# Performance work log

Hardware: AMD Instinct MI355X
Metric: run time of the kernel (lower is better)

Reference implementation:

```python
import jax, jax.numpy as jnp
import numpy as np

B, S, D = 4, 4096, 512
HEADS, NS, NEXT = 8, 32, 2048
HD = D // HEADS
SCALE = 1.0 / np.sqrt(HD)


def setup_inputs() -> dict:
    key = jax.random.key(0)
    ks = jax.random.split(key, 12)
    w_scale = 1.0 / np.sqrt(D)
    return {
        "sequence_tokens": jax.random.normal(ks[0], (B, S, D), jnp.float32),
        "sequence_mask": jnp.ones((B, S), dtype=bool),
        "ns_tokens": jax.random.normal(ks[1], (B, NS, D), jnp.float32),
        "ns_mask": jnp.ones((B, NS), dtype=bool),
        "next_sequence_length": NEXT,
        "Wq": jax.random.normal(ks[2], (D, D), jnp.float32) * w_scale,
        "Wk": jax.random.normal(ks[3], (D, D), jnp.float32) * w_scale,
        "Wv": jax.random.normal(ks[4], (D, D), jnp.float32) * w_scale,
        "ns_q_w": jax.random.normal(ks[5], (NS, D, D), jnp.float32) * w_scale,
        "ns_k_w": jax.random.normal(ks[6], (NS, D, D), jnp.float32) * w_scale,
        "ns_v_w": jax.random.normal(ks[7], (NS, D, D), jnp.float32) * w_scale,
        "Wo": jax.random.normal(ks[8], (D, D), jnp.float32) * w_scale,
    }


def reference(sequence_tokens, sequence_mask, ns_tokens, ns_mask,
              next_sequence_length, Wq, Wk, Wv, ns_q_w, ns_k_w, ns_v_w, Wo):
    b, s, d = sequence_tokens.shape
    ns = ns_tokens.shape[1]
    nxt = next_sequence_length

    seq_q = sequence_tokens[:, -nxt:]
    seq_q_mask = sequence_mask[:, -nxt:]

    # mixed projections: standard linear for seq tokens, per-position weights for NS tokens
    q = jnp.concatenate([seq_q @ Wq.T,
                         jnp.einsum('bnd,ndo->bno', ns_tokens, ns_q_w)], axis=1)
    k = jnp.concatenate([sequence_tokens @ Wk.T,
                         jnp.einsum('bnd,ndo->bno', ns_tokens, ns_k_w)], axis=1)
    v = jnp.concatenate([sequence_tokens @ Wv.T,
                         jnp.einsum('bnd,ndo->bno', ns_tokens, ns_v_w)], axis=1)

    def heads(x):  # [b, t, d] -> [b, h, t, hd]
        return x.reshape(b, -1, HEADS, HD).transpose(0, 2, 1, 3)
    q, k, v = heads(q), heads(k), heads(v)

    total = s + ns
    q_pos = jnp.concatenate([jnp.arange(s - nxt, s), jnp.arange(s, total)])
    k_pos = jnp.arange(total)
    causal = k_pos[None, :] <= q_pos[:, None]              # [Q, K]
    key_mask = jnp.concatenate([sequence_mask, ns_mask], axis=1)  # [b, K]

    logits = jnp.einsum('bhqd,bhkd->bhqk',
                        q.astype(jnp.float32), k.astype(jnp.float32)) * SCALE
    logits = jnp.where(causal[None, None], logits, -10000.0)
    logits = jnp.where(key_mask[:, None, None, :], logits, -10000.0)
    w = jax.nn.softmax(logits, axis=-1).astype(q.dtype)

    att = jnp.einsum('bhqk,bhkd->bhqd', w, v)
    att = att.transpose(0, 2, 1, 3).reshape(b, nxt + ns, d)
    att = att @ Wo.T

    seq_out = att[:, :nxt] * seq_q_mask[..., None].astype(att.dtype)
    ns_out = att[:, nxt:] * ns_mask[..., None].astype(att.dtype)
    return (seq_out, ns_out)
```

## Files before the change

### kernel.cpp

```cpp
#include <hip/hip_runtime.h>

#define NBATCH 4
#define SEQ    4096
#define DMODEL 512
#define NHEAD  8
#define HDIM   64
#define NSN    32
#define NXT    2048
#define QLEN   2080
#define KLEN   4128

using bf16x8 = __attribute__((ext_vector_type(8))) short;
using f32x4  = __attribute__((ext_vector_type(4))) float;

typedef __attribute__((address_space(1))) unsigned int gu32;
typedef __attribute__((address_space(3))) unsigned int lu32;

#define QSCALE 0.18033688f

__device__ __forceinline__ unsigned short f2bf(float f) {
  unsigned int u = __float_as_uint(f);
  u += 0x7FFF + ((u >> 16) & 1);
  return (unsigned short)(u >> 16);
}

__device__ __forceinline__ float bf2f(unsigned short u) {
  return __uint_as_float((unsigned int)u << 16);
}

__device__ __forceinline__ f32x4 mfma16(bf16x8 a, bf16x8 b, f32x4 c) {
  return __builtin_amdgcn_mfma_f32_16x16x32_bf16(a, b, c, 0, 0, 0);
}

__device__ __forceinline__ void gload_lds16(const void* g, void* lds_base) {
  __builtin_amdgcn_global_load_lds((const gu32*)g, (lu32*)lds_base, 16, 0, 0);
}

__device__ __forceinline__ unsigned int cvt_pk_bf16(float lo, float hi) {
  unsigned int r;
  asm("v_cvt_pk_bf16_f32 %0, %1, %2" : "=v"(r) : "v"(lo), "v"(hi));
  return r;
}

__global__ __launch_bounds__(256) void cvt_f32_bf16_v4(const float* __restrict__ src,
                                                       unsigned short* __restrict__ dst, int n4) {
  int i = blockIdx.x * 256 + threadIdx.x;
  if (i >= n4) return;
  float4 v = reinterpret_cast<const float4*>(src)[i];
  ushort4 r;
  r.x = f2bf(v.x); r.y = f2bf(v.y); r.z = f2bf(v.z); r.w = f2bf(v.w);
  reinterpret_cast<ushort4*>(dst)[i] = r;
}

__global__ __launch_bounds__(256) void cvt_w4(const float* __restrict__ a, const float* __restrict__ b,
                                              const float* __restrict__ c, const float* __restrict__ d,
                                              unsigned short* __restrict__ dst) {
  const float* s = blockIdx.y == 0 ? a : blockIdx.y == 1 ? b : blockIdx.y == 2 ? c : d;
  int i = blockIdx.x * 256 + threadIdx.x;
  float4 v = reinterpret_cast<const float4*>(s)[i];
  ushort4 r;
  r.x = f2bf(v.x); r.y = f2bf(v.y); r.z = f2bf(v.z); r.w = f2bf(v.w);
  reinterpret_cast<ushort4*>(dst)[(size_t)blockIdx.y * 65536 + i] = r;
}

__global__ __launch_bounds__(256) void proj_gemm(const unsigned short* __restrict__ X,
                                                 const unsigned short* __restrict__ W,
                                                 unsigned short* __restrict__ Out,
                                                 int rpb_shift, int row_off, int out_L, float scale) {
  __shared__ unsigned short As[128 * 32];
  __shared__ unsigned short Bs[128 * 32];
  const int tid = threadIdx.x;
  const int w = tid >> 6, l = tid & 63;
  const int lg = l >> 4, lr = l & 15;
  const int row0 = blockIdx.x * 128, col0 = blockIdx.y * 128;
  const int wr = (w >> 1) * 64, wc = (w & 1) * 64;
  const int mask = (1 << rpb_shift) - 1;

  f32x4 acc[4][4];
#pragma unroll
  for (int m = 0; m < 4; ++m)
#pragma unroll
    for (int n = 0; n < 4; ++n) acc[m][n] = (f32x4){0.f, 0.f, 0.f, 0.f};

  const int sr = w * 16 + (l >> 2);
  const int sc = (l & 3) * 8;

  for (int k0 = 0; k0 < 512; k0 += 32) {
#pragma unroll
    for (int i = 0; i < 2; ++i) {
      int gr = row0 + sr + i * 64;
      int xrow = ((gr >> rpb_shift) << 12) + row_off + (gr & mask);
      const unsigned short* gpa = X + (size_t)xrow * 512 + k0 + sc;
      gload_lds16(gpa, (char*)As + i * 4096 + w * 1024);
      const unsigned short* gpb = W + (size_t)(col0 + sr + i * 64) * 512 + k0 + sc;
      gload_lds16(gpb, (char*)Bs + i * 4096 + w * 1024);
    }
    __syncthreads();
    bf16x8 av[4], bv[4];
#pragma unroll
    for (int m = 0; m < 4; ++m) av[m] = *(const bf16x8*)&As[(wr + m * 16 + lr) * 32 + lg * 8];
#pragma unroll
    for (int n = 0; n < 4; ++n) bv[n] = *(const bf16x8*)&Bs[(wc + n * 16 + lr) * 32 + lg * 8];
#pragma unroll
    for (int m = 0; m < 4; ++m)
#pragma unroll
      for (int n = 0; n < 4; ++n) acc[m][n] = mfma16(av[m], bv[n], acc[m][n]);
    __syncthreads();
  }

#pragma unroll
  for (int m = 0; m < 4; ++m) {
    int crow = row0 + wr + m * 16 + lg * 4;
#pragma unroll
    for (int n = 0; n < 4; ++n) {
      int ccol = col0 + wc + n * 16 + lr;
      int hh = ccol >> 6, dd = ccol & 63;
#pragma unroll
      for (int r = 0; r < 4; ++r) {
        int cr = crow + r;
        int bb = cr >> rpb_shift, ii = cr & mask;
        Out[(((size_t)bb * NHEAD + hh) * out_L + ii) * HDIM + dd] = f2bf(acc[m][n][r] * scale);
      }
    }
  }
}

__global__ __launch_bounds__(256) void ns_proj(const float* __restrict__ nst,
                                               const float* __restrict__ Wnq, const float* __restrict__ Wnk,
                                               const float* __restrict__ Wnv,
                                               unsigned short* __restrict__ Qb, unsigned short* __restrict__ Kb,
                                               unsigned short* __restrict__ Vb) {
  const int oc = blockIdx.x, n = blockIdx.y, p = blockIdx.z;
  const float* W = p == 0 ? Wnq : p == 1 ? Wnk : Wnv;
  unsigned short* Out = p == 0 ? Qb : p == 1 ? Kb : Vb;
  const int out_L = p == 0 ? QLEN : KLEN;
  const int orow = p == 0 ? NXT + n : SEQ + n;
  const float scale = p == 0 ? QSCALE : 1.f;

  __shared__ float xs[NBATCH][DMODEL];
  __shared__ float red[NBATCH][128];
  const int tid = threadIdx.x;
  for (int idx = tid; idx < NBATCH * DMODEL; idx += 256)
    xs[idx >> 9][idx & 511] = nst[(size_t)((idx >> 9) * NSN + n) * DMODEL + (idx & 511)];
  __syncthreads();

  const int o = oc * 128 + (tid & 127);
  const int dh = tid >> 7;
  float a0 = 0.f, a1 = 0.f, a2 = 0.f, a3 = 0.f;
  const float* wp = W + (size_t)n * DMODEL * DMODEL + o;
#pragma unroll 8
  for (int d = dh * 256; d < dh * 256 + 256; ++d) {
    float wv = wp[(size_t)d * DMODEL];
    a0 += xs[0][d] * wv; a1 += xs[1][d] * wv; a2 += xs[2][d] * wv; a3 += xs[3][d] * wv;
  }
  if (dh == 1) { red[0][tid & 127] = a0; red[1][tid & 127] = a1; red[2][tid & 127] = a2; red[3][tid & 127] = a3; }
  __syncthreads();
  if (dh == 0) {
    a0 += red[0][tid & 127]; a1 += red[1][tid & 127]; a2 += red[2][tid & 127]; a3 += red[3][tid & 127];
    int hh = o >> 6, dd = o & 63;
    float v[4] = {a0, a1, a2, a3};
#pragma unroll
    for (int b = 0; b < NBATCH; ++b)
      Out[(((size_t)b * NHEAD + hh) * out_L + orow) * HDIM + dd] = f2bf(v[b] * scale);
  }
}

__global__ __launch_bounds__(256) void vtrans(const unsigned short* __restrict__ V,
                                              unsigned short* __restrict__ Vt) {
  __shared__ unsigned short t[64 * 64];
  const int tid = threadIdx.x;
  const int kv0 = blockIdx.x * 64, bh = blockIdx.y;
  const unsigned short* Vhp = V + (size_t)bh * KLEN * HDIM;
  unsigned short* Vtp = Vt + (size_t)bh * HDIM * KLEN;

#pragma unroll
  for (int i = 0; i < 2; ++i) {
    int c = i * 256 + tid;
    int row = c >> 3, c8 = c & 7;
    int kvg = kv0 + row; if (kvg > KLEN - 1) kvg = KLEN - 1;
    int4 v4 = *(const int4*)(Vhp + (size_t)kvg * HDIM + c8 * 8);
    *(int4*)&t[row * 64 + ((c8 ^ ((row >> 3) & 7)) * 8)] = v4;
  }
  __syncthreads();
#pragma unroll
  for (int i = 0; i < 2; ++i) {
    int c = i * 256 + tid;
    int d = c >> 3, k8 = c & 7;
    if (kv0 + k8 * 8 <= KLEN - 8) {
      unsigned int wd[4];
#pragma unroll
      for (int jj = 0; jj < 4; ++jj) {
        int ka = k8 * 8 + jj * 2, kb2 = ka + 1;
        unsigned int lo = t[ka  * 64 + (((d >> 3) ^ ((ka  >> 3) & 7)) * 8) + (d & 7)];
        unsigned int hi = t[kb2 * 64 + (((d >> 3) ^ ((kb2 >> 3) & 7)) * 8) + (d & 7)];
        wd[jj] = lo | (hi << 16);
      }
      int4 o; o.x = wd[0]; o.y = wd[1]; o.z = wd[2]; o.w = wd[3];
      *(int4*)(Vtp + (size_t)d * KLEN + kv0 + k8 * 8) = o;
    }
  }
}

__global__ __launch_bounds__(256) void attn_kernel(const unsigned short* __restrict__ Qb,
                                                   const unsigned short* __restrict__ Kb,
                                                   const unsigned short* __restrict__ Vtg,
                                                   unsigned short* __restrict__ PoA,
                                                   float2* __restrict__ PmlA,
                                                   unsigned short* __restrict__ PoB,
                                                   float2* __restrict__ PmlB) {
  __shared__ unsigned short Ks[64 * 64];
  __shared__ unsigned short Vs[64 * 64];

  const int tid = threadIdx.x;
  const int w = tid >> 6, l = tid & 63;
  const int lg = l >> 4, lr = l & 15;
  const bool geven = (l & 16) == 0;
  const int bx = (int)blockIdx.x;
  const int qb = 32 - bx / 3;
  const int sp = bx - 3 * (32 - qb);
  const int bh = (int)blockIdx.z * NHEAD + (int)blockIdx.y;
  const int q0 = qb * 64;
  const int base = NXT + q0;
  const int nkb = (base >> 6) + 1;
  const int t0 = (sp * nkb) / 3;
  const int t1 = ((sp + 1) * nkb) / 3;

  const unsigned short* Qh = Qb + (size_t)bh * QLEN * HDIM;
  const unsigned short* Kh = Kb + (size_t)bh * KLEN * HDIM;
  const unsigned short* Vh = Vtg + (size_t)bh * HDIM * KLEN;

  int qrow = q0 + w * 16 + lr; if (qrow > QLEN - 1) qrow = QLEN - 1;
  const bf16x8 qa0 = *(const bf16x8*)(Qh + (size_t)qrow * HDIM + lg * 8);
  const bf16x8 qa1 = *(const bf16x8*)(Qh + (size_t)qrow * HDIM + 32 + lg * 8);

  f32x4 acc[4];
#pragma unroll
  for (int n = 0; n < 4; ++n) acc[n] = (f32x4){0.f, 0.f, 0.f, 0.f};
  float m_r = 0.f, lsum = 0.f;

  const bf16x8 ones = {(short)0x3F80, (short)0x3F80, (short)0x3F80, (short)0x3F80,
                       (short)0x3F80, (short)0x3F80, (short)0x3F80, (short)0x3F80};

  const int rloc = l >> 3;
  const int jsrc = ((l & 7) ^ rloc) * 8;

  for (int kb = t0; kb < t1; ++kb) {
    const int kv0 = kb * 64;
    if (kv0 + 64 <= KLEN) {
#pragma unroll
      for (int i = 0; i < 2; ++i) {
        const int r8 = (w * 2 + i) * 8;
        gload_lds16(Kh + (size_t)(kv0 + r8 + rloc) * HDIM + jsrc, &Ks[r8 * 64]);
        gload_lds16(Vh + (size_t)(r8 + rloc) * KLEN + kv0 + jsrc, &Vs[r8 * 64]);
      }
    } else {
#pragma unroll
      for (int i = 0; i < 2; ++i) {
        const int r8 = (w * 2 + i) * 8;
        int kr = kv0 + r8 + rloc; if (kr > KLEN - 1) kr = KLEN - 1;
        gload_lds16(Kh + (size_t)kr * HDIM + jsrc, &Ks[r8 * 64]);
        int vc = kv0 + jsrc; if (vc > KLEN - 8) vc = KLEN - 8;
        gload_lds16(Vh + (size_t)(r8 + rloc) * KLEN + vc, &Vs[r8 * 64]);
      }
    }
    __syncthreads();

    const f32x4 minit = {-m_r, -m_r, -m_r, -m_r};
    f32x4 s[4];
#pragma unroll
    for (int n = 0; n < 4; ++n) {
      const int rk = n * 16 + lr;
      const bf16x8 k0 = *(const bf16x8*)&Ks[rk * 64 + ((lg ^ (rk & 7)) * 8)];
      const bf16x8 k1 = *(const bf16x8*)&Ks[rk * 64 + (((4 + lg) ^ (rk & 7)) * 8)];
      s[n] = mfma16(k0, qa0, minit);
      s[n] = mfma16(k1, qa1, s[n]);
    }

    if (kb == nkb - 1) {
      const int qk_lim = base + w * 16 + lr;
#pragma unroll
      for (int n = 0; n < 4; ++n)
#pragma unroll
        for (int r = 0; r < 4; ++r)
          if (kv0 + n * 16 + lg * 4 + r > qk_lim) s[n][r] = -1e30f;
    }

    float a3 = fmaxf(fmaxf(s[0][0], s[0][1]), s[0][2]);
    float b3 = fmaxf(fmaxf(s[0][3], s[1][0]), s[1][1]);
    float c3 = fmaxf(fmaxf(s[1][2], s[1][3]), s[2][0]);
    float d3 = fmaxf(fmaxf(s[2][1], s[2][2]), s[2][3]);
    float e3 = fmaxf(fmaxf(s[3][0], s[3][1]), s[3][2]);
    float rl = fmaxf(fmaxf(a3, b3), c3);
    rl = fmaxf(fmaxf(rl, d3), e3);
    rl = fmaxf(rl, s[3][3]);

    if (__any(rl > 11.5f)) {
      float rmax = fmaxf(rl, __shfl_xor(rl, 16));
      rmax = fmaxf(rmax, __shfl_xor(rmax, 32));
      float dl = fmaxf(rmax, 0.f);
      float sc = exp2f(-dl);
      lsum *= sc; m_r += dl;
#pragma unroll
      for (int n = 0; n < 4; ++n) {
        acc[n][0] *= sc; acc[n][1] *= sc; acc[n][2] *= sc; acc[n][3] *= sc;
#pragma unroll
        for (int r = 0; r < 4; ++r) s[n][r] = exp2f(s[n][r] - dl);
      }
    } else {
#pragma unroll
      for (int n = 0; n < 4; ++n)
#pragma unroll
        for (int r = 0; r < 4; ++r) s[n][r] = exp2f(s[n][r]);
    }

    unsigned int wpk[4][2];
#pragma unroll
    for (int n = 0; n < 4; ++n) {
      wpk[n][0] = cvt_pk_bf16(s[n][0], s[n][1]);
      wpk[n][1] = cvt_pk_bf16(s[n][2], s[n][3]);
    }
    bf16x8 pb[2];
#pragma unroll
    for (int ks = 0; ks < 2; ++ks) {
      unsigned int A0 = wpk[2 * ks][0], B0 = wpk[2 * ks + 1][0];
      unsigned int A1 = wpk[2 * ks][1], B1 = wpk[2 * ks + 1][1];
      asm("v_permlane32_swap_b32 %0, %1" : "+v"(A0), "+v"(B0));
      asm("v_permlane32_swap_b32 %0, %1" : "+v"(A1), "+v"(B1));
      unsigned int sA0 = __builtin_amdgcn_ds_swizzle(A0, 0x401F);
      unsigned int sA1 = __builtin_amdgcn_ds_swizzle(A1, 0x401F);
      unsigned int sB0 = __builtin_amdgcn_ds_swizzle(B0, 0x401F);
      unsigned int sB1 = __builtin_amdgcn_ds_swizzle(B1, 0x401F);
      int4 words;
      words.x = geven ? A0 : sB0;
      words.y = geven ? A1 : sB1;
      words.z = geven ? sA0 : B0;
      words.w = geven ? sA1 : B1;
      pb[ks] = *(bf16x8*)&words;
    }

    f32x4 acc_s = (f32x4){0.f, 0.f, 0.f, 0.f};
    acc_s = mfma16(ones, pb[0], acc_s);
    acc_s = mfma16(ones, pb[1], acc_s);
    lsum += acc_s[0];

#pragma unroll
    for (int n = 0; n < 4; ++n) {
      const int rv = n * 16 + lr;
#pragma unroll
      for (int ks = 0; ks < 2; ++ks) {
        const bf16x8 vv = *(const bf16x8*)&Vs[rv * 64 + (((ks * 4 + lg) ^ (rv & 7)) * 8)];
        acc[n] = mfma16(vv, pb[ks], acc[n]);
      }
    }

    __syncthreads();
  }

  const int qi = q0 + w * 16 + lr;
  if (qi < QLEN) {
    unsigned short* po; float2* pml; size_t rowp;
    if (sp < 2) { rowp = (size_t)(sp * 32 + bh) * QLEN + qi; po = PoA + rowp * 64; pml = PmlA + rowp; }
    else        { rowp = (size_t)bh * QLEN + qi;             po = PoB + rowp * 64; pml = PmlB + rowp; }
#pragma unroll
    for (int n = 0; n < 4; ++n) {
      ushort4 pk;
      pk.x = f2bf(acc[n][0]); pk.y = f2bf(acc[n][1]);
      pk.z = f2bf(acc[n][2]); pk.w = f2bf(acc[n][3]);
      *(ushort4*)(po + n * 16 + lg * 4) = pk;
    }
    if (l < 16) *pml = (float2){m_r, lsum};
  }
}

__global__ __launch_bounds__(256) void attn_combine(const unsigned short* __restrict__ PoA,
                                                    const float2* __restrict__ PmlA,
                                                    const unsigned short* __restrict__ PoB,
                                                    const float2* __restrict__ PmlB,
                                                    unsigned short* __restrict__ Att) {
  const int bh = blockIdx.y;
  const int idx = blockIdx.x * 256 + threadIdx.x;
  const int qi = idx >> 3, dc = (idx & 7) * 8;
  const size_t row = (size_t)bh * QLEN + qi;
  const float2 ml0 = PmlA[row];
  const float2 ml1 = PmlA[(size_t)32 * QLEN + row];
  const float2 ml2 = PmlB[row];
  const float mm = fmaxf(fmaxf(ml0.x, ml1.x), ml2.x);
  float s0 = exp2f(ml0.x - mm), s1 = exp2f(ml1.x - mm), s2 = exp2f(ml2.x - mm);
  const float inv = 1.f / (ml0.y * s0 + ml1.y * s1 + ml2.y * s2);
  s0 *= inv; s1 *= inv; s2 *= inv;
  const bf16x8 o0 = *(const bf16x8*)(PoA + row * 64 + dc);
  const bf16x8 o1 = *(const bf16x8*)(PoA + ((size_t)32 * QLEN + row) * 64 + dc);
  const bf16x8 o2 = *(const bf16x8*)(PoB + row * 64 + dc);
  unsigned short out[8];
#pragma unroll
  for (int j = 0; j < 8; ++j)
    out[j] = f2bf(bf2f((unsigned short)o0[j]) * s0 + bf2f((unsigned short)o1[j]) * s1 +
                  bf2f((unsigned short)o2[j]) * s2);
  const int b = bh >> 3, h = bh & 7;
  *(int4*)(Att + ((size_t)b * QLEN + qi) * DMODEL + h * HDIM + dc) = *(int4*)out;
}

__global__ __launch_bounds__(256) void out_gemm(const unsigned short* __restrict__ A,
                                                const unsigned short* __restrict__ W,
                                                float* __restrict__ Out) {
  __shared__ unsigned short As[128 * 32];
  __shared__ unsigned short Bs[128 * 32];
  const int tid = threadIdx.x;
  const int w = tid >> 6, l = tid & 63;
  const int lg = l >> 4, lr = l & 15;
  const int row0 = blockIdx.x * 128, col0 = blockIdx.y * 128;
  const int wr = (w >> 1) * 64, wc = (w & 1) * 64;

  f32x4 acc[4][4];
#pragma unroll
  for (int m = 0; m < 4; ++m)
#pragma unroll
    for (int n = 0; n < 4; ++n) acc[m][n] = (f32x4){0.f, 0.f, 0.f, 0.f};

  const int sr = w * 16 + (l >> 2);
  const int sc = (l & 3) * 8;

  for (int k0 = 0; k0 < 512; k0 += 32) {
#pragma unroll
    for (int i = 0; i < 2; ++i) {
      const unsigned short* gpa = A + (size_t)(row0 + sr + i * 64) * 512 + k0 + sc;
      gload_lds16(gpa, (char*)As + i * 4096 + w * 1024);
      const unsigned short* gpb = W + (size_t)(col0 + sr + i * 64) * 512 + k0 + sc;
      gload_lds16(gpb, (char*)Bs + i * 4096 + w * 1024);
    }
    __syncthreads();
    bf16x8 av[4], bv[4];
#pragma unroll
    for (int m = 0; m < 4; ++m) av[m] = *(const bf16x8*)&As[(wr + m * 16 + lr) * 32 + lg * 8];
#pragma unroll
    for (int n = 0; n < 4; ++n) bv[n] = *(const bf16x8*)&Bs[(wc + n * 16 + lr) * 32 + lg * 8];
#pragma unroll
    for (int m = 0; m < 4; ++m)
#pragma unroll
      for (int n = 0; n < 4; ++n) acc[m][n] = mfma16(av[m], bv[n], acc[m][n]);
    __syncthreads();
  }

#pragma unroll
  for (int m = 0; m < 4; ++m) {
    int crow = row0 + wr + m * 16 + lg * 4;
#pragma unroll
    for (int n = 0; n < 4; ++n) {
      int ccol = col0 + wc + n * 16 + lr;
#pragma unroll
      for (int r = 0; r < 4; ++r) {
        int cr = crow + r;
        int bb = cr / QLEN, ii = cr - bb * QLEN;
        size_t off = ii < NXT
                       ? ((size_t)bb * NXT + ii) * DMODEL + ccol
                       : (size_t)NBATCH * NXT * DMODEL + ((size_t)bb * NSN + (ii - NXT)) * DMODEL + ccol;
        Out[off] = acc[m][n][r];
      }
    }
  }
}

extern "C" void kernel_launch(void* const* d_in, const int* in_sizes, int n_in,
                              void* d_out, int out_size, void* d_ws, size_t ws_size,
                              hipStream_t stream) {
  const float* seq = (const float*)d_in[0];
  const float* nst = (const float*)d_in[2];
  const float* Wq  = (const float*)d_in[5];
  const float* Wk  = (const float*)d_in[6];
  const float* Wv  = (const float*)d_in[7];
  const float* nsq = (const float*)d_in[8];
  const float* nsk = (const float*)d_in[9];
  const float* nsv = (const float*)d_in[10];
  const float* Wo  = (const float*)d_in[11];
  float* out = (float*)d_out;

  char* ws = (char*)d_ws;
  unsigned short* Xbf  = (unsigned short*)(ws);
  unsigned short* Wqb  = (unsigned short*)(ws + 16777216);
  unsigned short* Wkb  = Wqb + 262144;
  unsigned short* Wvb  = Wkb + 262144;
  unsigned short* Wob  = Wvb + 262144;
  unsigned short* Qbuf = (unsigned short*)(ws + 18874368);
  unsigned short* Kbuf = (unsigned short*)(ws + 27394048);
  unsigned short* Vbuf = (unsigned short*)(ws + 44302336);
  unsigned short* Att  = (unsigned short*)(ws + 61210624);
  unsigned short* Vtg  = (unsigned short*)(ws + 69730304);
  unsigned short* PoA  = (unsigned short*)(ws);
  float2*         PmlA = (float2*)(ws + 17039360);
  unsigned short* PoB  = (unsigned short*)(ws + 44302336);
  float2*         PmlB = (float2*)(ws + 52822016);
  if (ws_size < 86638592) return;

  cvt_f32_bf16_v4<<<dim3(8192), dim3(256), 0, stream>>>(seq, Xbf, 2097152);
  cvt_w4<<<dim3(256, 4), dim3(256), 0, stream>>>(Wq, Wk, Wv, Wo, Wqb);
  proj_gemm<<<dim3(128, 4), dim3(256), 0, stream>>>(Xbf, Wkb, Kbuf, 12, 0, KLEN, 1.f);
  proj_gemm<<<dim3(128, 4), dim3(256), 0, stream>>>(Xbf, Wvb, Vbuf, 12, 0, KLEN, 1.f);
  proj_gemm<<<dim3(64, 4), dim3(256), 0, stream>>>(Xbf, Wqb, Qbuf, 11, 2048, QLEN, QSCALE);
  ns_proj<<<dim3(4, 32, 3), dim3(256), 0, stream>>>(nst, nsq, nsk, nsv, Qbuf, Kbuf, Vbuf);
  vtrans<<<dim3(65, 32), dim3(256), 0, stream>>>(Vbuf, Vtg);
  attn_kernel<<<dim3(99, 8, 4), dim3(256), 0, stream>>>(Qbuf, Kbuf, Vtg, PoA, PmlA, PoB, PmlB);
  attn_combine<<<dim3(65, 32), dim3(256), 0, stream>>>(PoA, PmlA, PoB, PmlB, Att);
  out_gemm<<<dim3(65, 4), dim3(256), 0, stream>>>(Att, Wob, out);
}
```

Measured before the change: 227.1 us.

## Process two query tiles per wave to reuse K/V tiles in attention

Each attention block now covers 128 query rows instead of 64, with each wave holding two 16-row Q tiles. Every K/V tile loaded into shared memory therefore feeds twice as many MFMAs, which halves K/V global traffic and the number of blocks (grid 99 to 51 in x). It also keeps per-tile running max and sum statistics, switches to incremental load pointers, and adds a waves-per-EU hint. The cost is higher register pressure and fewer blocks, which may lower occupancy and load balance across the diagonal causal tiles.

```diff
diff --git a/kernel.cpp b/kernel.cpp
--- a/kernel.cpp
+++ b/kernel.cpp
@@ -201,13 +201,15 @@
   }
 }
 
-__global__ __launch_bounds__(256) void attn_kernel(const unsigned short* __restrict__ Qb,
-                                                   const unsigned short* __restrict__ Kb,
-                                                   const unsigned short* __restrict__ Vtg,
-                                                   unsigned short* __restrict__ PoA,
-                                                   float2* __restrict__ PmlA,
-                                                   unsigned short* __restrict__ PoB,
-                                                   float2* __restrict__ PmlB) {
+__global__ __launch_bounds__(256)
+__attribute__((amdgpu_waves_per_eu(1, 4)))
+void attn_kernel(const unsigned short* __restrict__ Qb,
+                 const unsigned short* __restrict__ Kb,
+                 const unsigned short* __restrict__ Vtg,
+                 unsigned short* __restrict__ PoA,
+                 float2* __restrict__ PmlA,
+                 unsigned short* __restrict__ PoB,
+                 float2* __restrict__ PmlB) {
   __shared__ unsigned short Ks[64 * 64];
   __shared__ unsigned short Vs[64 * 64];
 
@@ -216,12 +218,13 @@
   const int lg = l >> 4, lr = l & 15;
   const bool geven = (l & 16) == 0;
   const int bx = (int)blockIdx.x;
-  const int qb = 32 - bx / 3;
-  const int sp = bx - 3 * (32 - qb);
+  const int qb = 16 - bx / 3;
+  const int sp = bx - 3 * (16 - qb);
   const int bh = (int)blockIdx.z * NHEAD + (int)blockIdx.y;
-  const int q0 = qb * 64;
+  const int q0 = qb * 128;
   const int base = NXT + q0;
-  const int nkb = (base >> 6) + 1;
+  int nkb = (base >> 6) + 2; if (nkb > 65) nkb = 65;
+  const int kbm = base >> 6;
   const int t0 = (sp * nkb) / 3;
   const int t1 = ((sp + 1) * nkb) / 3;
 
@@ -229,119 +232,166 @@
   const unsigned short* Kh = Kb + (size_t)bh * KLEN * HDIM;
   const unsigned short* Vh = Vtg + (size_t)bh * HDIM * KLEN;
 
-  int qrow = q0 + w * 16 + lr; if (qrow > QLEN - 1) qrow = QLEN - 1;
-  const bf16x8 qa0 = *(const bf16x8*)(Qh + (size_t)qrow * HDIM + lg * 8);
-  const bf16x8 qa1 = *(const bf16x8*)(Qh + (size_t)qrow * HDIM + 32 + lg * 8);
-
-  f32x4 acc[4];
-#pragma unroll
-  for (int n = 0; n < 4; ++n) acc[n] = (f32x4){0.f, 0.f, 0.f, 0.f};
-  float m_r = 0.f, lsum = 0.f;
+  bf16x8 qa[2][2];
+#pragma unroll
+  for (int qt = 0; qt < 2; ++qt) {
+    int qrow = q0 + w * 32 + qt * 16 + lr; if (qrow > QLEN - 1) qrow = QLEN - 1;
+    qa[qt][0] = *(const bf16x8*)(Qh + (size_t)qrow * HDIM + lg * 8);
+    qa[qt][1] = *(const bf16x8*)(Qh + (size_t)qrow * HDIM + 32 + lg * 8);
+  }
+
+  f32x4 acc0[4], acc1[4];
+#pragma unroll
+  for (int n = 0; n < 4; ++n) {
+    acc0[n] = (f32x4){0.f, 0.f, 0.f, 0.f};
+    acc1[n] = (f32x4){0.f, 0.f, 0.f, 0.f};
+  }
+  float m_r[2] = {0.f, 0.f}, lsum[2] = {0.f, 0.f};
+  f32x4 mini[2] = {(f32x4){0.f, 0.f, 0.f, 0.f}, (f32x4){0.f, 0.f, 0.f, 0.f}};
 
   const bf16x8 ones = {(short)0x3F80, (short)0x3F80, (short)0x3F80, (short)0x3F80,
                        (short)0x3F80, (short)0x3F80, (short)0x3F80, (short)0x3F80};
 
   const int rloc = l >> 3;
   const int jsrc = ((l & 7) ^ rloc) * 8;
+  const int r8a = (w * 2) * 8, r8b = (w * 2 + 1) * 8;
+  const unsigned short* kpa = Kh + (size_t)(t0 * 64 + r8a + rloc) * HDIM + jsrc;
+  const unsigned short* kpb = Kh + (size_t)(t0 * 64 + r8b + rloc) * HDIM + jsrc;
+  const unsigned short* vpa = Vh + (size_t)(r8a + rloc) * KLEN + t0 * 64 + jsrc;
+  const unsigned short* vpb = Vh + (size_t)(r8b + rloc) * KLEN + t0 * 64 + jsrc;
 
   for (int kb = t0; kb < t1; ++kb) {
-    const int kv0 = kb * 64;
-    if (kv0 + 64 <= KLEN) {
+    if (kb != 64) {
+      gload_lds16(kpa, &Ks[r8a * 64]);
+      gload_lds16(kpb, &Ks[r8b * 64]);
+      gload_lds16(vpa, &Vs[r8a * 64]);
+      gload_lds16(vpb, &Vs[r8b * 64]);
+      kpa += 64 * HDIM; kpb += 64 * HDIM; vpa += 64; vpb += 64;
+    } else {
 #pragma unroll
       for (int i = 0; i < 2; ++i) {
         const int r8 = (w * 2 + i) * 8;
-        gload_lds16(Kh + (size_t)(kv0 + r8 + rloc) * HDIM + jsrc, &Ks[r8 * 64]);
-        gload_lds16(Vh + (size_t)(r8 + rloc) * KLEN + kv0 + jsrc, &Vs[r8 * 64]);
-      }
-    } else {
-#pragma unroll
-      for (int i = 0; i < 2; ++i) {
-        const int r8 = (w * 2 + i) * 8;
-        int kr = kv0 + r8 + rloc; if (kr > KLEN - 1) kr = KLEN - 1;
+        int kr = 4096 + r8 + rloc; if (kr > KLEN - 1) kr = KLEN - 1;
         gload_lds16(Kh + (size_t)kr * HDIM + jsrc, &Ks[r8 * 64]);
-        int vc = kv0 + jsrc; if (vc > KLEN - 8) vc = KLEN - 8;
+        int vc = 4096 + jsrc; if (vc > KLEN - 8) vc = KLEN - 8;
         gload_lds16(Vh + (size_t)(r8 + rloc) * KLEN + vc, &Vs[r8 * 64]);
       }
     }
     __syncthreads();
 
-    const f32x4 minit = {-m_r, -m_r, -m_r, -m_r};
-    f32x4 s[4];
+    const int kv0 = kb * 64;
+
+    f32x4 s0[4], s1[4];
 #pragma unroll
     for (int n = 0; n < 4; ++n) {
       const int rk = n * 16 + lr;
       const bf16x8 k0 = *(const bf16x8*)&Ks[rk * 64 + ((lg ^ (rk & 7)) * 8)];
       const bf16x8 k1 = *(const bf16x8*)&Ks[rk * 64 + (((4 + lg) ^ (rk & 7)) * 8)];
-      s[n] = mfma16(k0, qa0, minit);
-      s[n] = mfma16(k1, qa1, s[n]);
-    }
-
-    if (kb == nkb - 1) {
-      const int qk_lim = base + w * 16 + lr;
+      s0[n] = mfma16(k0, qa[0][0], mini[0]);
+      s0[n] = mfma16(k1, qa[0][1], s0[n]);
+      s1[n] = mfma16(k0, qa[1][0], mini[1]);
+      s1[n] = mfma16(k1, qa[1][1], s1[n]);
+    }
+
+    if (kb >= kbm) {
+      const int qp0 = base + w * 32 + lr;
+      const int qp1 = qp0 + 16;
+#pragma unroll
+      for (int n = 0; n < 4; ++n) {
+        const int kvb = kv0 + n * 16 + lg * 4;
+#pragma unroll
+        for (int r = 0; r < 4; ++r) {
+          if (kvb + r > qp0) s0[n][r] = -1e30f;
+          if (kvb + r > qp1) s1[n][r] = -1e30f;
+        }
+      }
+    }
+
+    float x0 = fmaxf(fmaxf(s0[0][0], s0[0][1]), s0[0][2]);
+    float x1 = fmaxf(fmaxf(s0[0][3], s0[1][0]), s0[1][1]);
+    float x2 = fmaxf(fmaxf(s0[1][2], s0[1][3]), s0[2][0]);
+    float x3 = fmaxf(fmaxf(s0[2][1], s0[2][2]), s0[2][3]);
+    float x4 = fmaxf(fmaxf(s0[3][0], s0[3][1]), s0[3][2]);
+    float x5 = fmaxf(fmaxf(s0[3][3], s1[0][0]), s1[0][1]);
+    float x6 = fmaxf(fmaxf(s1[0][2], s1[0][3]), s1[1][0]);
+    float x7 = fmaxf(fmaxf(s1[1][1], s1[1][2]), s1[1][3]);
+    float x8 = fmaxf(fmaxf(s1[2][0], s1[2][1]), s1[2][2]);
+    float x9 = fmaxf(fmaxf(s1[2][3], s1[3][0]), s1[3][1]);
+    float rl = fmaxf(fmaxf(x0, x1), x2);
+    rl = fmaxf(fmaxf(rl, x3), x4);
+    rl = fmaxf(fmaxf(rl, x5), x6);
+    rl = fmaxf(fmaxf(rl, x7), x8);
+    rl = fmaxf(fmaxf(rl, x9), fmaxf(s1[3][2], s1[3][3]));
+
+    if (__any(rl > 11.5f)) {
+      float rm0 = fmaxf(fmaxf(fmaxf(x0, x1), x2), fmaxf(fmaxf(x3, x4), s0[3][3]));
+      float rm1 = fmaxf(fmaxf(fmaxf(fmaxf(s1[0][0], s1[0][1]), fmaxf(s1[0][2], s1[0][3])), x7),
+                        fmaxf(fmaxf(x8, x9), fmaxf(fmaxf(s1[1][0], s1[3][2]), s1[3][3])));
+      rm0 = fmaxf(rm0, __shfl_xor(rm0, 16)); rm0 = fmaxf(rm0, __shfl_xor(rm0, 32));
+      rm1 = fmaxf(rm1, __shfl_xor(rm1, 16)); rm1 = fmaxf(rm1, __shfl_xor(rm1, 32));
+      float dl0 = fmaxf(rm0, 0.f), dl1 = fmaxf(rm1, 0.f);
+      float sc0 = exp2f(-dl0), sc1 = exp2f(-dl1);
+      lsum[0] *= sc0; lsum[1] *= sc1;
+      m_r[0] += dl0; m_r[1] += dl1;
+      mini[0] = (f32x4){-m_r[0], -m_r[0], -m_r[0], -m_r[0]};
+      mini[1] = (f32x4){-m_r[1], -m_r[1], -m_r[1], -m_r[1]};
+#pragma unroll
+      for (int n = 0; n < 4; ++n) {
+#pragma unroll
+        for (int r = 0; r < 4; ++r) {
+          acc0[n][r] *= sc0; acc1[n][r] *= sc1;
+          s0[n][r] = exp2f(s0[n][r] - dl0);
+          s1[n][r] = exp2f(s1[n][r] - dl1);
+        }
+      }
+    } else {
 #pragma unroll
       for (int n = 0; n < 4; ++n)
 #pragma unroll
-        for (int r = 0; r < 4; ++r)
-          if (kv0 + n * 16 + lg * 4 + r > qk_lim) s[n][r] = -1e30f;
-    }
-
-    float a3 = fmaxf(fmaxf(s[0][0], s[0][1]), s[0][2]);
-    float b3 = fmaxf(fmaxf(s[0][3], s[1][0]), s[1][1]);
-    float c3 = fmaxf(fmaxf(s[1][2], s[1][3]), s[2][0]);
-    float d3 = fmaxf(fmaxf(s[2][1], s[2][2]), s[2][3]);
-    float e3 = fmaxf(fmaxf(s[3][0], s[3][1]), s[3][2]);
-    float rl = fmaxf(fmaxf(a3, b3), c3);
-    rl = fmaxf(fmaxf(rl, d3), e3);
-    rl = fmaxf(rl, s[3][3]);
-
-    if (__any(rl > 11.5f)) {
-      float rmax = fmaxf(rl, __shfl_xor(rl, 16));
-      rmax = fmaxf(rmax, __shfl_xor(rmax, 32));
-      float dl = fmaxf(rmax, 0.f);
-      float sc = exp2f(-dl);
-      lsum *= sc; m_r += dl;
+        for (int r = 0; r < 4; ++r) {
+          s0[n][r] = exp2f(s0[n][r]);
+          s1[n][r] = exp2f(s1[n][r]);
+        }
+    }
+
+    bf16x8 pb0[2], pb1[2];
+#pragma unroll
+    for (int qt = 0; qt < 2; ++qt) {
+      f32x4* s = qt ? s1 : s0;
+      unsigned int wpk[4][2];
 #pragma unroll
       for (int n = 0; n < 4; ++n) {
-        acc[n][0] *= sc; acc[n][1] *= sc; acc[n][2] *= sc; acc[n][3] *= sc;
-#pragma unroll
-        for (int r = 0; r < 4; ++r) s[n][r] = exp2f(s[n][r] - dl);
-      }
-    } else {
-#pragma unroll
-      for (int n = 0; n < 4; ++n)
-#pragma unroll
-        for (int r = 0; r < 4; ++r) s[n][r] = exp2f(s[n][r]);
-    }
-
-    unsigned int wpk[4][2];
-#pragma unroll
-    for (int n = 0; n < 4; ++n) {
-      wpk[n][0] = cvt_pk_bf16(s[n][0], s[n][1]);
-      wpk[n][1] = cvt_pk_bf16(s[n][2], s[n][3]);
-    }
-    bf16x8 pb[2];
-#pragma unroll
-    for (int ks = 0; ks < 2; ++ks) {
-      unsigned int A0 = wpk[2 * ks][0], B0 = wpk[2 * ks + 1][0];
-      unsigned int A1 = wpk[2 * ks][1], B1 = wpk[2 * ks + 1][1];
-      asm("v_permlane32_swap_b32 %0, %1" : "+v"(A0), "+v"(B0));
-      asm("v_permlane32_swap_b32 %0, %1" : "+v"(A1), "+v"(B1));
-      unsigned int sA0 = __builtin_amdgcn_ds_swizzle(A0, 0x401F);
-      unsigned int sA1 = __builtin_amdgcn_ds_swizzle(A1, 0x401F);
-      unsigned int sB0 = __builtin_amdgcn_ds_swizzle(B0, 0x401F);
-      unsigned int sB1 = __builtin_amdgcn_ds_swizzle(B1, 0x401F);
-      int4 words;
-      words.x = geven ? A0 : sB0;
-      words.y = geven ? A1 : sB1;
-      words.z = geven ? sA0 : B0;
-      words.w = geven ? sA1 : B1;
-      pb[ks] = *(bf16x8*)&words;
-    }
-
-    f32x4 acc_s = (f32x4){0.f, 0.f, 0.f, 0.f};
-    acc_s = mfma16(ones, pb[0], acc_s);
-    acc_s = mfma16(ones, pb[1], acc_s);
-    lsum += acc_s[0];
+        wpk[n][0] = cvt_pk_bf16(s[n][0], s[n][1]);
+        wpk[n][1] = cvt_pk_bf16(s[n][2], s[n][3]);
+      }
+      bf16x8* pb = qt ? pb1 : pb0;
+#pragma unroll
+      for (int ks = 0; ks < 2; ++ks) {
+        unsigned int A0 = wpk[2 * ks][0], B0 = wpk[2 * ks + 1][0];
+        unsigned int A1 = wpk[2 * ks][1], B1 = wpk[2 * ks + 1][1];
+        asm("v_permlane32_swap_b32 %0, %1" : "+v"(A0), "+v"(B0));
+        asm("v_permlane32_swap_b32 %0, %1" : "+v"(A1), "+v"(B1));
+        unsigned int sA0 = __builtin_amdgcn_ds_swizzle(A0, 0x401F);
+        unsigned int sA1 = __builtin_amdgcn_ds_swizzle(A1, 0x401F);
+        unsigned int sB0 = __builtin_amdgcn_ds_swizzle(B0, 0x401F);
+        unsigned int sB1 = __builtin_amdgcn_ds_swizzle(B1, 0x401F);
+        int4 words;
+        words.x = geven ? A0 : sB0;
+        words.y = geven ? A1 : sB1;
+        words.z = geven ? sA0 : B0;
+        words.w = geven ? sA1 : B1;
+        pb[ks] = *(bf16x8*)&words;
+      }
+    }
+
+    f32x4 as0 = (f32x4){0.f, 0.f, 0.f, 0.f};
+    as0 = mfma16(ones, pb0[0], as0);
+    as0 = mfma16(ones, pb0[1], as0);
+    lsum[0] += as0[0];
+    f32x4 as1 = (f32x4){0.f, 0.f, 0.f, 0.f};
+    as1 = mfma16(ones, pb1[0], as1);
+    as1 = mfma16(ones, pb1[1], as1);
+    lsum[1] += as1[0];
 
 #pragma unroll
     for (int n = 0; n < 4; ++n) {
@@ -349,26 +399,31 @@
 #pragma unroll
       for (int ks = 0; ks < 2; ++ks) {
         const bf16x8 vv = *(const bf16x8*)&Vs[rv * 64 + (((ks * 4 + lg) ^ (rv & 7)) * 8)];
-        acc[n] = mfma16(vv, pb[ks], acc[n]);
+        acc0[n] = mfma16(vv, pb0[ks], acc0[n]);
+        acc1[n] = mfma16(vv, pb1[ks], acc1[n]);
       }
     }
 
     __syncthreads();
   }
 
-  const int qi = q0 + w * 16 + lr;
-  if (qi < QLEN) {
-    unsigned short* po; float2* pml; size_t rowp;
-    if (sp < 2) { rowp = (size_t)(sp * 32 + bh) * QLEN + qi; po = PoA + rowp * 64; pml = PmlA + rowp; }
-    else        { rowp = (size_t)bh * QLEN + qi;             po = PoB + rowp * 64; pml = PmlB + rowp; }
-#pragma unroll
-    for (int n = 0; n < 4; ++n) {
-      ushort4 pk;
-      pk.x = f2bf(acc[n][0]); pk.y = f2bf(acc[n][1]);
-      pk.z = f2bf(acc[n][2]); pk.w = f2bf(acc[n][3]);
-      *(ushort4*)(po + n * 16 + lg * 4) = pk;
-    }
-    if (l < 16) *pml = (float2){m_r, lsum};
+#pragma unroll
+  for (int qt = 0; qt < 2; ++qt) {
+    const int qi = q0 + w * 32 + qt * 16 + lr;
+    if (qi < QLEN) {
+      f32x4* acc = qt ? acc1 : acc0;
+      unsigned short* po; float2* pml; size_t rowp;
+      if (sp < 2) { rowp = (size_t)(sp * 32 + bh) * QLEN + qi; po = PoA + rowp * 64; pml = PmlA + rowp; }
+      else        { rowp = (size_t)bh * QLEN + qi;             po = PoB + rowp * 64; pml = PmlB + rowp; }
+#pragma unroll
+      for (int n = 0; n < 4; ++n) {
+        ushort4 pk;
+        pk.x = f2bf(acc[n][0]); pk.y = f2bf(acc[n][1]);
+        pk.z = f2bf(acc[n][2]); pk.w = f2bf(acc[n][3]);
+        *(ushort4*)(po + n * 16 + lg * 4) = pk;
+      }
+      if (l < 16) *pml = (float2){m_r[qt], lsum[qt]};
+    }
   }
 }
 
@@ -498,7 +553,7 @@
   proj_gemm<<<dim3(64, 4), dim3(256), 0, stream>>>(Xbf, Wqb, Qbuf, 11, 2048, QLEN, QSCALE);
   ns_proj<<<dim3(4, 32, 3), dim3(256), 0, stream>>>(nst, nsq, nsk, nsv, Qbuf, Kbuf, Vbuf);
   vtrans<<<dim3(65, 32), dim3(256), 0, stream>>>(Vbuf, Vtg);
-  attn_kernel<<<dim3(99, 8, 4), dim3(256), 0, stream>>>(Qbuf, Kbuf, Vtg, PoA, PmlA, PoB, PmlB);
+  attn_kernel<<<dim3(51, 8, 4), dim3(256), 0, stream>>>(Qbuf, Kbuf, Vtg, PoA, PmlA, PoB, PmlB);
   attn_combine<<<dim3(65, 32), dim3(256), 0, stream>>>(PoA, PmlA, PoB, PmlB, Att);
   out_gemm<<<dim3(65, 4), dim3(256), 0, stream>>>(Att, Wob, out);
 }
```

Measured after the change: 256.8 us. 13.1% more time.

## Double-buffer K/V tiles in LDS to overlap loads with attention compute

Applied to the files above, without the earlier changes.

The attention kernel now keeps two LDS buffers each for K and V. The next key block is issued as an asynchronous global-to-LDS load before the current block's QK, softmax and PV work runs. This is meant to hide global load latency behind MFMA work, and it drops one barrier per iteration. The cost is doubled LDS use per block, which could lower the number of resident blocks per CU.

```diff
diff --git a/kernel.cpp b/kernel.cpp
--- a/kernel.cpp
+++ b/kernel.cpp
@@ -208,8 +208,8 @@
                                                    float2* __restrict__ PmlA,
                                                    unsigned short* __restrict__ PoB,
                                                    float2* __restrict__ PmlB) {
-  __shared__ unsigned short Ks[64 * 64];
-  __shared__ unsigned short Vs[64 * 64];
+  __shared__ unsigned short Ks[2][64 * 64];
+  __shared__ unsigned short Vs[2][64 * 64];
 
   const int tid = threadIdx.x;
   const int w = tid >> 6, l = tid & 63;
@@ -244,34 +244,47 @@
   const int rloc = l >> 3;
   const int jsrc = ((l & 7) ^ rloc) * 8;
 
+#define STAGE(buf, kv0s)                                                            \
+  {                                                                                 \
+    if ((kv0s) + 64 <= KLEN) {                                                      \
+      _Pragma("unroll")                                                             \
+      for (int i = 0; i < 2; ++i) {                                                 \
+        const int r8 = (w * 2 + i) * 8;                                             \
+        gload_lds16(Kh + (size_t)((kv0s) + r8 + rloc) * HDIM + jsrc,                \
+                    &Ks[buf][r8 * 64]);                                             \
+        gload_lds16(Vh + (size_t)(r8 + rloc) * KLEN + (kv0s) + jsrc,                \
+                    &Vs[buf][r8 * 64]);                                             \
+      }                                                                             \
+    } else {                                                                        \
+      _Pragma("unroll")                                                             \
+      for (int i = 0; i < 2; ++i) {                                                 \
+        const int r8 = (w * 2 + i) * 8;                                             \
+        int kr = (kv0s) + r8 + rloc; if (kr > KLEN - 1) kr = KLEN - 1;              \
+        gload_lds16(Kh + (size_t)kr * HDIM + jsrc, &Ks[buf][r8 * 64]);              \
+        int vc = (kv0s) + jsrc; if (vc > KLEN - 8) vc = KLEN - 8;                   \
+        gload_lds16(Vh + (size_t)(r8 + rloc) * KLEN + vc, &Vs[buf][r8 * 64]);       \
+      }                                                                             \
+    }                                                                               \
+  }
+
+  STAGE(0, t0 * 64)
+  __syncthreads();
+  int cur = 0;
+
   for (int kb = t0; kb < t1; ++kb) {
+    if (kb + 1 < t1) STAGE(cur ^ 1, (kb + 1) * 64)
+
+    const unsigned short* Kc = &Ks[cur][0];
+    const unsigned short* Vc = &Vs[cur][0];
     const int kv0 = kb * 64;
-    if (kv0 + 64 <= KLEN) {
-#pragma unroll
-      for (int i = 0; i < 2; ++i) {
-        const int r8 = (w * 2 + i) * 8;
-        gload_lds16(Kh + (size_t)(kv0 + r8 + rloc) * HDIM + jsrc, &Ks[r8 * 64]);
-        gload_lds16(Vh + (size_t)(r8 + rloc) * KLEN + kv0 + jsrc, &Vs[r8 * 64]);
-      }
-    } else {
-#pragma unroll
-      for (int i = 0; i < 2; ++i) {
-        const int r8 = (w * 2 + i) * 8;
-        int kr = kv0 + r8 + rloc; if (kr > KLEN - 1) kr = KLEN - 1;
-        gload_lds16(Kh + (size_t)kr * HDIM + jsrc, &Ks[r8 * 64]);
-        int vc = kv0 + jsrc; if (vc > KLEN - 8) vc = KLEN - 8;
-        gload_lds16(Vh + (size_t)(r8 + rloc) * KLEN + vc, &Vs[r8 * 64]);
-      }
-    }
-    __syncthreads();
 
     const f32x4 minit = {-m_r, -m_r, -m_r, -m_r};
     f32x4 s[4];
 #pragma unroll
     for (int n = 0; n < 4; ++n) {
       const int rk = n * 16 + lr;
-      const bf16x8 k0 = *(const bf16x8*)&Ks[rk * 64 + ((lg ^ (rk & 7)) * 8)];
-      const bf16x8 k1 = *(const bf16x8*)&Ks[rk * 64 + (((4 + lg) ^ (rk & 7)) * 8)];
+      const bf16x8 k0 = *(const bf16x8*)&Kc[rk * 64 + ((lg ^ (rk & 7)) * 8)];
+      const bf16x8 k1 = *(const bf16x8*)&Kc[rk * 64 + (((4 + lg) ^ (rk & 7)) * 8)];
       s[n] = mfma16(k0, qa0, minit);
       s[n] = mfma16(k1, qa1, s[n]);
     }
@@ -348,12 +361,13 @@
       const int rv = n * 16 + lr;
 #pragma unroll
       for (int ks = 0; ks < 2; ++ks) {
-        const bf16x8 vv = *(const bf16x8*)&Vs[rv * 64 + (((ks * 4 + lg) ^ (rv & 7)) * 8)];
+        const bf16x8 vv = *(const bf16x8*)&Vc[rv * 64 + (((ks * 4 + lg) ^ (rv & 7)) * 8)];
         acc[n] = mfma16(vv, pb[ks], acc[n]);
       }
     }
 
     __syncthreads();
+    cur ^= 1;
   }
 
   const int qi = q0 + w * 16 + lr;
@@ -370,6 +384,7 @@
     }
     if (l < 16) *pml = (float2){m_r, lsum};
   }
+#undef STAGE
 }
 
 __global__ __launch_bounds__(256) void attn_combine(const unsigned short* __restrict__ PoA,
```

Result: no change. 230.2 us (+1.4%).
